# Performance work log

Measured on AMD Instinct MI355X. Metric: run time of the kernel, lower is better.

The kernel has to match this reference:

```python
import jax, jax.numpy as jnp
import numpy as np

O, A, H, L = 32, 8, 256, 3   # obs_units, act_units, hidden_units, hidden_layers
SCALE = 1.0                  # obs_scale
N, W = 512, 128              # n obs/action rows, n hypernet weight samples
W_TOTAL = (O*H + H) + (A*H + H) + (2*H*H + H) + L*(H*H + H) + (H*O + O) + (H + 1) + (H + 1)  # 348194


def _unpack(w):
    # Slice the flat per-sample weight vector exactly as PrimaryNetwork.feedforward does.
    c = [0]
    def take(n, shape=None):
        s = w[:, c[0]:c[0]+n]
        c[0] += n
        return s.reshape((w.shape[0],) + shape) if shape is not None else s
    w_obs = take(O*H, (H, O)); b_obs = take(H)
    w_act = take(A*H, (H, A)); b_act = take(H)
    w_tgt = take(2*H*H, (H, 2*H)); b_tgt = take(H)
    ws, bs = [], []
    for _ in range(L):
        ws.append(take(H*H, (H, H))); bs.append(take(H))
    w_state = take(H*O, (O, H)); b_state = take(O)
    w_reward = take(H, (1, H)); b_reward = take(1)
    w_done = take(H, (1, H)); b_done = take(1)
    return w_obs, b_obs, w_act, b_act, w_tgt, b_tgt, ws, bs, w_state, b_state, w_reward, b_reward, w_done, b_done


def setup_inputs() -> dict:
    key = jax.random.key(0)
    k1, k2, k3 = jax.random.split(key, 3)
    return {
        "obs": jax.random.normal(k1, (N, O), jnp.float32),
        "action": jax.random.normal(k2, (N, A), jnp.float32),
        # scale ~1/sqrt(H) so activations stay in a sane range through the MLP
        "w": jax.random.normal(k3, (W, W_TOTAL), jnp.float32) * (1.0 / np.sqrt(H)),
        "obs_min": jnp.zeros((O,), jnp.float32),
        "obs_max": jnp.ones((O,), jnp.float32),
    }


def reference(obs, action, w, obs_min, obs_max):
    lrelu = jax.nn.leaky_relu  # negative_slope=0.01, matches F.leaky_relu default
    (w_obs, b_obs, w_act, b_act, w_tgt, b_tgt, ws, bs,
     w_state, b_state, w_reward, b_reward, w_done, b_done) = _unpack(w)

    # normalize obs to [-scale, scale]
    x = (obs - obs_min[None, :]) / (obs_max - obs_min)[None, :]
    x = (2.0 * x - 1.0) * SCALE                         # [N, O]

    # per-sample hypernetwork MLP, batched over (N obs rows) x (W weight samples)
    o = jnp.einsum('who,no->nwh', w_obs, x) + b_obs[None]          # [N, W, H]
    a = jnp.einsum('wha,na->nwh', w_act, action) + b_act[None]     # [N, W, H]
    y = lrelu(jnp.concatenate([o, a], axis=-1))                    # [N, W, 2H]
    y = lrelu(jnp.einsum('whk,nwk->nwh', w_tgt, y) + b_tgt[None])  # [N, W, H]
    for wj, bj in zip(ws, bs):
        y = lrelu(jnp.einsum('whk,nwk->nwh', wj, y) + bj[None])

    next_states = jnp.einsum('wok,nwk->nwo', w_state, y) + b_state[None] + x[:, None, :]  # [N, W, O]
    rewards = jnp.tanh(jnp.einsum('wok,nwk->nwo', w_reward, y) + b_reward[None])          # [N, W, 1]
    dones = jax.nn.sigmoid(jnp.einsum('wok,nwk->nwo', w_done, y) + b_done[None])          # [N, W, 1]

    # un-normalize next_states
    next_states = (next_states / SCALE + 1.0) * 0.5
    next_states = next_states * (obs_max - obs_min)[None, None, :] + obs_min[None, None, :]
    return next_states, rewards, dones
```

## Files before the change

kernel.cpp:

```cpp
#include <hip/hip_runtime.h>
#include <cstdint>
#include <cstddef>

#define NMEM    128
#define WTOTAL  348194

#define OFF_WOBS   0
#define OFF_BOBS   8192
#define OFF_WACT   8448
#define OFF_BACT   10496
#define OFF_WTGT   10752
#define OFF_BTGT   141824
#define OFF_WS0    142080
#define OFF_BS0    207616
#define OFF_WS1    207872
#define OFF_BS1    273408
#define OFF_WS2    273664
#define OFF_BS2    339200
#define OFF_WSTATE 339456
#define OFF_BSTATE 347648
#define OFF_WREW   347680
#define OFF_BREW   347936
#define OFF_WDONE  347937
#define OFF_BDONE  348193

#define OUT_REW  2097152
#define OUT_DONE 2162688

#define RB 128
#define APITCH 264

typedef __attribute__((ext_vector_type(8))) short short8;
typedef __attribute__((ext_vector_type(4))) float f32x4;

__device__ __forceinline__ uint32_t pkbf2(float lo, float hi) {
  union { float f; uint32_t u; } a, b;
  a.f = lo; b.f = hi;
  return __builtin_amdgcn_perm(b.u + 0x8000u, a.u + 0x8000u, 0x07060302u);
}

__device__ __forceinline__ uint16_t f2b_fast(float f) {
  union { float f; uint32_t u; } x; x.f = f;
  return (uint16_t)((x.u + 0x8000u) >> 16);
}

__device__ __forceinline__ short8 pk8(const float2 f[4]) {
  union { uint32_t u[4]; short8 s; } r;
#pragma unroll
  for (int i = 0; i < 4; ++i) r.u[i] = pkbf2(f[i].x, f[i].y);
  return r.s;
}

__device__ __forceinline__ void zero8(f32x4 acc[8]) {
#pragma unroll
  for (int r = 0; r < 8; ++r)
#pragma unroll
    for (int j = 0; j < 4; ++j) acc[r][j] = 0.0f;
}

__device__ __forceinline__ void accum_k8(f32x4 acc[8],
                                         const uint16_t* __restrict__ Ab,
                                         const float* __restrict__ wrow) {
  float2 f[2][4];
#pragma unroll
  for (int i = 0; i < 4; ++i)
    f[0][i] = reinterpret_cast<const float2*>(wrow)[i];
#pragma unroll
  for (int kt = 0; kt < 8; ++kt) {
    if (kt < 7) {
#pragma unroll
      for (int i = 0; i < 4; ++i)
        f[(kt + 1) & 1][i] =
            reinterpret_cast<const float2*>(wrow + (kt + 1) * 32)[i];
    }
    const short8 b = pk8(f[kt & 1]);
#pragma unroll
    for (int rt = 0; rt < 8; ++rt) {
      const short8 a =
          *reinterpret_cast<const short8*>(Ab + rt * 16 * APITCH + kt * 32);
      acc[rt] = __builtin_amdgcn_mfma_f32_16x16x32_bf16(a, b, acc[rt], 0, 0, 0);
    }
  }
}

__device__ __forceinline__ void epi_lrelu(const f32x4 acc[8], float bv,
                                          uint16_t* __restrict__ B, int c,
                                          int lg) {
#pragma unroll
  for (int rt = 0; rt < 8; ++rt) {
#pragma unroll
    for (int j = 0; j < 4; ++j) {
      float v = acc[rt][j] + bv;
      v = (v > 0.0f) ? v : 0.01f * v;
      B[(rt * 16 + lg * 4 + j) * APITCH + c] = f2b_fast(v);
    }
  }
}

__global__ void __launch_bounds__(1024, 8)
pn_kernel(const float* __restrict__ obs, const float* __restrict__ action,
          const float* __restrict__ w, const float* __restrict__ omin,
          const float* __restrict__ omax, float* __restrict__ out)
{
  __shared__ __align__(16) uint16_t B1[RB * APITCH];

  const int tid  = threadIdx.x;
  const int lane = tid & 63;
  const int wid  = tid >> 6;
  const int lr   = lane & 15;
  const int lg   = lane >> 4;
  const int c    = wid * 16 + lr;

  const int bid    = blockIdx.x;
  const int xcd    = bid & 7;
  const int j5     = bid >> 3;
  const int member = xcd * 16 + (j5 >> 2);
  const int chunk  = j5 & 3;
  const int n0     = chunk * RB;
  const float* wm  = w + (size_t)member * WTOTAL;

  const uint16_t* Ab = B1 + lr * APITCH + lg * 8;

  {
    float sc[8], of[8];
#pragma unroll
    for (int i = 0; i < 8; ++i) {
      const float mn = omin[lg * 8 + i], mx = omax[lg * 8 + i];
      const float s = 2.0f / (mx - mn);
      sc[i] = s;
      of[i] = -mn * s - 1.0f;
    }
    float2 fb[4];
#pragma unroll
    for (int i = 0; i < 4; ++i)
      fb[i] = reinterpret_cast<const float2*>(wm + OFF_WOBS + c * 32 + lg * 8)[i];
    const short8 b = pk8(fb);
    const float bb = wm[OFF_BOBS + c];
#pragma unroll
    for (int rt = 0; rt < 8; ++rt) {
      const int n = n0 + rt * 16 + lr;
      const float4 x0 = *reinterpret_cast<const float4*>(obs + n * 32 + lg * 8);
      const float4 x1 = *reinterpret_cast<const float4*>(obs + n * 32 + lg * 8 + 4);
      union { uint32_t u[4]; short8 s; } afr;
      afr.u[0] = pkbf2(x0.x * sc[0] + of[0], x0.y * sc[1] + of[1]);
      afr.u[1] = pkbf2(x0.z * sc[2] + of[2], x0.w * sc[3] + of[3]);
      afr.u[2] = pkbf2(x1.x * sc[4] + of[4], x1.y * sc[5] + of[5]);
      afr.u[3] = pkbf2(x1.z * sc[6] + of[6], x1.w * sc[7] + of[7]);
      f32x4 a0 = {0.0f, 0.0f, 0.0f, 0.0f};
      a0 = __builtin_amdgcn_mfma_f32_16x16x32_bf16(afr.s, b, a0, 0, 0, 0);
#pragma unroll
      for (int j = 0; j < 4; ++j) {
        float v = a0[j] + bb;
        v = (v > 0.0f) ? v : 0.01f * v;
        B1[(rt * 16 + lg * 4 + j) * APITCH + c] = f2b_fast(v);
      }
    }
  }
  __syncthreads();

  f32x4 acc[8];
  zero8(acc);

  accum_k8(acc, Ab, wm + OFF_WTGT + c * 512 + lg * 8);
  __syncthreads();

  {
    float2 fb[4];
#pragma unroll
    for (int i = 0; i < 4; ++i)
      fb[i] = reinterpret_cast<const float2*>(wm + OFF_WACT + c * 8 + lg * 8)[i];
    const short8 b = pk8(fb);
    const float bb = wm[OFF_BACT + c];
#pragma unroll
    for (int rt = 0; rt < 8; ++rt) {
      const int n = n0 + rt * 16 + lr;
      union { uint32_t u[4]; short8 s; } afr;
      if (lg == 0) {
        const float4 q0 = *reinterpret_cast<const float4*>(action + n * 8);
        const float4 q1 = *reinterpret_cast<const float4*>(action + n * 8 + 4);
        afr.u[0] = pkbf2(q0.x, q0.y);
        afr.u[1] = pkbf2(q0.z, q0.w);
        afr.u[2] = pkbf2(q1.x, q1.y);
        afr.u[3] = pkbf2(q1.z, q1.w);
      } else {
        afr.u[0] = afr.u[1] = afr.u[2] = afr.u[3] = 0u;
      }
      f32x4 a0 = {0.0f, 0.0f, 0.0f, 0.0f};
      a0 = __builtin_amdgcn_mfma_f32_16x16x32_bf16(afr.s, b, a0, 0, 0, 0);
#pragma unroll
      for (int j = 0; j < 4; ++j) {
        float v = a0[j] + bb;
        v = (v > 0.0f) ? v : 0.01f * v;
        B1[(rt * 16 + lg * 4 + j) * APITCH + c] = f2b_fast(v);
      }
    }
  }
  __syncthreads();

  accum_k8(acc, Ab, wm + OFF_WTGT + c * 512 + 256 + lg * 8);
  __syncthreads();
  epi_lrelu(acc, wm[OFF_BTGT + c], B1, c, lg);
  __syncthreads();

  zero8(acc);
  accum_k8(acc, Ab, wm + OFF_WS0 + c * 256 + lg * 8);
  __syncthreads();
  epi_lrelu(acc, wm[OFF_BS0 + c], B1, c, lg);
  __syncthreads();

  zero8(acc);
  accum_k8(acc, Ab, wm + OFF_WS1 + c * 256 + lg * 8);
  __syncthreads();
  epi_lrelu(acc, wm[OFF_BS1 + c], B1, c, lg);
  __syncthreads();

  zero8(acc);
  accum_k8(acc, Ab, wm + OFF_WS2 + c * 256 + lg * 8);
  __syncthreads();
  epi_lrelu(acc, wm[OFF_BS2 + c], B1, c, lg);
  __syncthreads();

  if (wid < 3) {
    zero8(acc);
#pragma unroll
    for (int kt = 0; kt < 8; ++kt) {
      short8 b;
      if (c < 32) {
        const float* p = wm + OFF_WSTATE + c * 256 + kt * 32 + lg * 8;
        float2 f[4];
#pragma unroll
        for (int i = 0; i < 4; ++i) f[i] = reinterpret_cast<const float2*>(p)[i];
        b = pk8(f);
      } else if (c == 32) {
        const float* p = wm + OFF_WREW + kt * 32 + lg * 8;
        float2 f[4];
#pragma unroll
        for (int i = 0; i < 4; ++i) f[i] = reinterpret_cast<const float2*>(p)[i];
        b = pk8(f);
      } else if (c == 33) {
        const float* p = wm + OFF_WDONE + kt * 32 + lg * 8;
        union { uint32_t u[4]; short8 s; } r;
#pragma unroll
        for (int i = 0; i < 4; ++i) r.u[i] = pkbf2(p[2 * i], p[2 * i + 1]);
        b = r.s;
      } else {
        union { uint32_t u[4]; short8 s; } z;
        z.u[0] = z.u[1] = z.u[2] = z.u[3] = 0u;
        b = z.s;
      }
#pragma unroll
      for (int rt = 0; rt < 8; ++rt) {
        const short8 a =
            *reinterpret_cast<const short8*>(Ab + rt * 16 * APITCH + kt * 32);
        acc[rt] = __builtin_amdgcn_mfma_f32_16x16x32_bf16(a, b, acc[rt], 0, 0, 0);
      }
    }

    if (c < 34) {
#pragma unroll
      for (int rt = 0; rt < 8; ++rt) {
#pragma unroll
        for (int j = 0; j < 4; ++j) {
          const int n = n0 + rt * 16 + lg * 4 + j;
          float v = acc[rt][j];
          if (c < 32) {
            const float mn = omin[c], mx = omax[c];
            const float rng = mx - mn;
            const float x = 2.0f * (obs[n * 32 + c] - mn) / rng - 1.0f;
            v += wm[OFF_BSTATE + c] + x;
            v = (v + 1.0f) * 0.5f;
            out[((size_t)n * NMEM + member) * 32 + c] = v * rng + mn;
          } else if (c == 32) {
            v += wm[OFF_BREW];
            out[(size_t)OUT_REW + (size_t)n * NMEM + member] = tanhf(v);
          } else {
            v += wm[OFF_BDONE];
            out[(size_t)OUT_DONE + (size_t)n * NMEM + member] =
                1.0f / (1.0f + expf(-v));
          }
        }
      }
    }
  }
}

extern "C" void kernel_launch(void* const* d_in, const int* in_sizes, int n_in,
                              void* d_out, int out_size, void* d_ws, size_t ws_size,
                              hipStream_t stream) {
  (void)in_sizes; (void)n_in; (void)out_size; (void)d_ws; (void)ws_size;
  const float* obs    = (const float*)d_in[0];
  const float* action = (const float*)d_in[1];
  const float* w      = (const float*)d_in[2];
  const float* omin   = (const float*)d_in[3];
  const float* omax   = (const float*)d_in[4];
  float* out = (float*)d_out;

  pn_kernel<<<dim3(512), dim3(1024), 0, stream>>>(obs, action, w, omin, omax, out);
}
```

Baseline: 135.7 us.

## Stage hidden-layer weights through double-buffered swizzled LDS with coalesced prefetch

Per-lane strided global loads of weight rows for each MFMA k-step are replaced by a cooperative, coalesced load of 64-wide K slices for all 256 output columns. Each slice is packed to bf16 and written into a double-buffered XOR-swizzled LDS tile, and the next slice (including the next layer's first slice) is prefetched while MFMAs consume the current one. This aims to cut global load inefficiency and latency stalls. In exchange it adds 64KB of LDS, a barrier per slice, and lowers the launch_bounds occupancy hint.

```diff
diff --git a/kernel.cpp b/kernel.cpp
--- a/kernel.cpp
+++ b/kernel.cpp
@@ -29,9 +29,11 @@
 
 #define RB 128
 #define APITCH 264
+#define WSN 16384
 
 typedef __attribute__((ext_vector_type(8))) short short8;
 typedef __attribute__((ext_vector_type(4))) float f32x4;
+typedef __attribute__((ext_vector_type(4))) unsigned int u32x4;
 
 __device__ __forceinline__ uint32_t pkbf2(float lo, float hi) {
   union { float f; uint32_t u; } a, b;
@@ -44,7 +46,7 @@
   return (uint16_t)((x.u + 0x8000u) >> 16);
 }
 
-__device__ __forceinline__ short8 pk8(const float2 f[4]) {
+__device__ __forceinline__ short8 pk8f2(const float2 f[4]) {
   union { uint32_t u[4]; short8 s; } r;
 #pragma unroll
   for (int i = 0; i < 4; ++i) r.u[i] = pkbf2(f[i].x, f[i].y);
@@ -58,28 +60,48 @@
     for (int j = 0; j < 4; ++j) acc[r][j] = 0.0f;
 }
 
-__device__ __forceinline__ void accum_k8(f32x4 acc[8],
-                                         const uint16_t* __restrict__ Ab,
-                                         const float* __restrict__ wrow) {
-  float2 f[2][4];
-#pragma unroll
-  for (int i = 0; i < 4; ++i)
-    f[0][i] = reinterpret_cast<const float2*>(wrow)[i];
-#pragma unroll
-  for (int kt = 0; kt < 8; ++kt) {
-    if (kt < 7) {
-#pragma unroll
-      for (int i = 0; i < 4; ++i)
-        f[(kt + 1) & 1][i] =
-            reinterpret_cast<const float2*>(wrow + (kt + 1) * 32)[i];
-    }
-    const short8 b = pk8(f[kt & 1]);
-#pragma unroll
-    for (int rt = 0; rt < 8; ++rt) {
-      const short8 a =
-          *reinterpret_cast<const short8*>(Ab + rt * 16 * APITCH + kt * 32);
-      acc[rt] = __builtin_amdgcn_mfma_f32_16x16x32_bf16(a, b, acc[rt], 0, 0, 0);
-    }
+__device__ __forceinline__ void ws_commit(const float2 g[8], uint16_t* wsb,
+                                          int wsoff0, int wsoff1) {
+  uint32_t d[8];
+#pragma unroll
+  for (int i = 0; i < 8; ++i) d[i] = pkbf2(g[i].x, g[i].y);
+  *reinterpret_cast<u32x4*>(wsb + wsoff0) = (u32x4){d[0], d[1], d[2], d[3]};
+  *reinterpret_cast<u32x4*>(wsb + wsoff1) = (u32x4){d[4], d[5], d[6], d[7]};
+}
+
+template <bool NX>
+__device__ __forceinline__ void accum_lds(f32x4 acc[8],
+                                          const uint16_t* __restrict__ Ab,
+                                          uint16_t* __restrict__ WS,
+                                          const float* __restrict__ sp,
+                                          const float* __restrict__ np,
+                                          int wsoff0, int wsoff1,
+                                          int wrd, int lrm, int lg) {
+#pragma unroll
+  for (int s = 0; s < 4; ++s) {
+    float2 g[8];
+    if (s < 3 || NX) {
+      const float* src = (s < 3) ? (sp + (s + 1) * 64) : np;
+#pragma unroll
+      for (int i = 0; i < 8; ++i)
+        g[i] = reinterpret_cast<const float2*>(src)[i];
+    }
+    const uint16_t* wsr = WS + (s & 1) * WSN + wrd;
+#pragma unroll
+    for (int h = 0; h < 2; ++h) {
+      const short8 b = *reinterpret_cast<const short8*>(
+          wsr + (((h * 4 + lg) ^ lrm) * 8));
+#pragma unroll
+      for (int rt = 0; rt < 8; ++rt) {
+        const short8 a = *reinterpret_cast<const short8*>(
+            Ab + rt * 16 * APITCH + (s * 2 + h) * 32);
+        acc[rt] =
+            __builtin_amdgcn_mfma_f32_16x16x32_bf16(a, b, acc[rt], 0, 0, 0);
+      }
+    }
+    if (s < 3 || NX)
+      ws_commit(g, WS + ((s + 1) & 1) * WSN, wsoff0, wsoff1);
+    __syncthreads();
   }
 }
 
@@ -97,12 +119,13 @@
   }
 }
 
-__global__ void __launch_bounds__(1024, 8)
+__global__ void __launch_bounds__(1024, 4)
 pn_kernel(const float* __restrict__ obs, const float* __restrict__ action,
           const float* __restrict__ w, const float* __restrict__ omin,
           const float* __restrict__ omax, float* __restrict__ out)
 {
   __shared__ __align__(16) uint16_t B1[RB * APITCH];
+  __shared__ __align__(16) uint16_t WS[2 * WSN];
 
   const int tid  = threadIdx.x;
   const int lane = tid & 63;
@@ -121,6 +144,23 @@
 
   const uint16_t* Ab = B1 + lr * APITCH + lg * 8;
 
+  const int scol   = tid >> 2;
+  const int spart  = tid & 3;
+  const int wsoff0 = scol * 64 + (((2 * spart)     ^ (scol & 7)) * 8);
+  const int wsoff1 = scol * 64 + (((2 * spart + 1) ^ (scol & 7)) * 8);
+  const float* sp_t1 = wm + OFF_WTGT + scol * 512 + spart * 16;
+  const float* sp_t2 = sp_t1 + 256;
+  const float* sp_h0 = wm + OFF_WS0 + scol * 256 + spart * 16;
+  const float* sp_h1 = wm + OFF_WS1 + scol * 256 + spart * 16;
+  const float* sp_h2 = wm + OFF_WS2 + scol * 256 + spart * 16;
+  const int wrd = c * 64;
+  const int lrm = lr & 7;
+
+  float2 gp[8];
+#pragma unroll
+  for (int i = 0; i < 8; ++i)
+    gp[i] = reinterpret_cast<const float2*>(sp_t1)[i];
+
   {
     float sc[8], of[8];
 #pragma unroll
@@ -134,7 +174,7 @@
 #pragma unroll
     for (int i = 0; i < 4; ++i)
       fb[i] = reinterpret_cast<const float2*>(wm + OFF_WOBS + c * 32 + lg * 8)[i];
-    const short8 b = pk8(fb);
+    const short8 b = pk8f2(fb);
     const float bb = wm[OFF_BOBS + c];
 #pragma unroll
     for (int rt = 0; rt < 8; ++rt) {
@@ -156,20 +196,20 @@
       }
     }
   }
+  ws_commit(gp, WS, wsoff0, wsoff1);
   __syncthreads();
 
   f32x4 acc[8];
   zero8(acc);
 
-  accum_k8(acc, Ab, wm + OFF_WTGT + c * 512 + lg * 8);
-  __syncthreads();
+  accum_lds<true>(acc, Ab, WS, sp_t1, sp_t2, wsoff0, wsoff1, wrd, lrm, lg);
 
   {
     float2 fb[4];
 #pragma unroll
     for (int i = 0; i < 4; ++i)
       fb[i] = reinterpret_cast<const float2*>(wm + OFF_WACT + c * 8 + lg * 8)[i];
-    const short8 b = pk8(fb);
+    const short8 b = pk8f2(fb);
     const float bb = wm[OFF_BACT + c];
 #pragma unroll
     for (int rt = 0; rt < 8; ++rt) {
@@ -197,26 +237,22 @@
   }
   __syncthreads();
 
-  accum_k8(acc, Ab, wm + OFF_WTGT + c * 512 + 256 + lg * 8);
-  __syncthreads();
+  accum_lds<true>(acc, Ab, WS, sp_t2, sp_h0, wsoff0, wsoff1, wrd, lrm, lg);
   epi_lrelu(acc, wm[OFF_BTGT + c], B1, c, lg);
   __syncthreads();
 
   zero8(acc);
-  accum_k8(acc, Ab, wm + OFF_WS0 + c * 256 + lg * 8);
-  __syncthreads();
+  accum_lds<true>(acc, Ab, WS, sp_h0, sp_h1, wsoff0, wsoff1, wrd, lrm, lg);
   epi_lrelu(acc, wm[OFF_BS0 + c], B1, c, lg);
   __syncthreads();
 
   zero8(acc);
-  accum_k8(acc, Ab, wm + OFF_WS1 + c * 256 + lg * 8);
-  __syncthreads();
+  accum_lds<true>(acc, Ab, WS, sp_h1, sp_h2, wsoff0, wsoff1, wrd, lrm, lg);
   epi_lrelu(acc, wm[OFF_BS1 + c], B1, c, lg);
   __syncthreads();
 
   zero8(acc);
-  accum_k8(acc, Ab, wm + OFF_WS2 + c * 256 + lg * 8);
-  __syncthreads();
+  accum_lds<false>(acc, Ab, WS, sp_h2, sp_h2, wsoff0, wsoff1, wrd, lrm, lg);
   epi_lrelu(acc, wm[OFF_BS2 + c], B1, c, lg);
   __syncthreads();
 
@@ -230,13 +266,13 @@
         float2 f[4];
 #pragma unroll
         for (int i = 0; i < 4; ++i) f[i] = reinterpret_cast<const float2*>(p)[i];
-        b = pk8(f);
+        b = pk8f2(f);
       } else if (c == 32) {
         const float* p = wm + OFF_WREW + kt * 32 + lg * 8;
         float2 f[4];
 #pragma unroll
         for (int i = 0; i < 4; ++i) f[i] = reinterpret_cast<const float2*>(p)[i];
-        b = pk8(f);
+        b = pk8f2(f);
       } else if (c == 33) {
         const float* p = wm + OFF_WDONE + kt * 32 + lg * 8;
         union { uint32_t u[4]; short8 s; } r;
```

Result: slower. 257.5 us (+89.8%).

## Double row tile to 256 per block and deepen weight prefetch

Applied to the files above, without the earlier changes.

Each block now processes 256 obs rows instead of 128 for one ensemble member, halving the grid to 256 blocks so each member's weights are loaded and converted to bf16 by two blocks rather than four. Accumulators double to 16 MFMA tiles per wave, and the weight loads for a layer are prefetched four k-steps ahead instead of one. The shared activation buffer doubles to about 135 KB and register pressure rises, which lowers occupancy; with 256 blocks there is only one block per CU on a 256-CU part, so latency hiding depends on within-wave ILP.

```diff
diff --git a/kernel.cpp b/kernel.cpp
--- a/kernel.cpp
+++ b/kernel.cpp
@@ -27,7 +27,7 @@
 #define OUT_REW  2097152
 #define OUT_DONE 2162688
 
-#define RB 128
+#define RB 256
 #define APITCH 264
 
 typedef __attribute__((ext_vector_type(8))) short short8;
@@ -44,38 +44,41 @@
   return (uint16_t)((x.u + 0x8000u) >> 16);
 }
 
-__device__ __forceinline__ short8 pk8(const float2 f[4]) {
+__device__ __forceinline__ short8 pk8f2(const float2 f[4]) {
   union { uint32_t u[4]; short8 s; } r;
 #pragma unroll
   for (int i = 0; i < 4; ++i) r.u[i] = pkbf2(f[i].x, f[i].y);
   return r.s;
 }
 
-__device__ __forceinline__ void zero8(f32x4 acc[8]) {
-#pragma unroll
-  for (int r = 0; r < 8; ++r)
+__device__ __forceinline__ void zero16(f32x4 acc[16]) {
+#pragma unroll
+  for (int r = 0; r < 16; ++r)
 #pragma unroll
     for (int j = 0; j < 4; ++j) acc[r][j] = 0.0f;
 }
 
-__device__ __forceinline__ void accum_k8(f32x4 acc[8],
-                                         const uint16_t* __restrict__ Ab,
-                                         const float* __restrict__ wrow) {
-  float2 f[2][4];
-#pragma unroll
-  for (int i = 0; i < 4; ++i)
-    f[0][i] = reinterpret_cast<const float2*>(wrow)[i];
+__device__ __forceinline__ void accum_pass(f32x4 acc[16],
+                                           const uint16_t* __restrict__ Ab,
+                                           const float* __restrict__ w0) {
+  float2 g[4][4];
+#pragma unroll
+  for (int d = 0; d < 4; ++d)
+#pragma unroll
+    for (int i = 0; i < 4; ++i)
+      g[d][i] = reinterpret_cast<const float2*>(w0 + d * 32)[i];
+
 #pragma unroll
   for (int kt = 0; kt < 8; ++kt) {
-    if (kt < 7) {
+    const int s = kt & 3;
+    const short8 b = pk8f2(g[s]);
+    if (kt < 4) {
 #pragma unroll
       for (int i = 0; i < 4; ++i)
-        f[(kt + 1) & 1][i] =
-            reinterpret_cast<const float2*>(wrow + (kt + 1) * 32)[i];
-    }
-    const short8 b = pk8(f[kt & 1]);
-#pragma unroll
-    for (int rt = 0; rt < 8; ++rt) {
+        g[s][i] = reinterpret_cast<const float2*>(w0 + (kt + 4) * 32)[i];
+    }
+#pragma unroll
+    for (int rt = 0; rt < 16; ++rt) {
       const short8 a =
           *reinterpret_cast<const short8*>(Ab + rt * 16 * APITCH + kt * 32);
       acc[rt] = __builtin_amdgcn_mfma_f32_16x16x32_bf16(a, b, acc[rt], 0, 0, 0);
@@ -83,11 +86,11 @@
   }
 }
 
-__device__ __forceinline__ void epi_lrelu(const f32x4 acc[8], float bv,
+__device__ __forceinline__ void epi_lrelu(const f32x4 acc[16], float bv,
                                           uint16_t* __restrict__ B, int c,
                                           int lg) {
 #pragma unroll
-  for (int rt = 0; rt < 8; ++rt) {
+  for (int rt = 0; rt < 16; ++rt) {
 #pragma unroll
     for (int j = 0; j < 4; ++j) {
       float v = acc[rt][j] + bv;
@@ -97,7 +100,7 @@
   }
 }
 
-__global__ void __launch_bounds__(1024, 8)
+__global__ void __launch_bounds__(1024, 4)
 pn_kernel(const float* __restrict__ obs, const float* __restrict__ action,
           const float* __restrict__ w, const float* __restrict__ omin,
           const float* __restrict__ omax, float* __restrict__ out)
@@ -114,8 +117,8 @@
   const int bid    = blockIdx.x;
   const int xcd    = bid & 7;
   const int j5     = bid >> 3;
-  const int member = xcd * 16 + (j5 >> 2);
-  const int chunk  = j5 & 3;
+  const int member = xcd * 16 + (j5 >> 1);
+  const int chunk  = j5 & 1;
   const int n0     = chunk * RB;
   const float* wm  = w + (size_t)member * WTOTAL;
 
@@ -134,10 +137,10 @@
 #pragma unroll
     for (int i = 0; i < 4; ++i)
       fb[i] = reinterpret_cast<const float2*>(wm + OFF_WOBS + c * 32 + lg * 8)[i];
-    const short8 b = pk8(fb);
+    const short8 b = pk8f2(fb);
     const float bb = wm[OFF_BOBS + c];
 #pragma unroll
-    for (int rt = 0; rt < 8; ++rt) {
+    for (int rt = 0; rt < 16; ++rt) {
       const int n = n0 + rt * 16 + lr;
       const float4 x0 = *reinterpret_cast<const float4*>(obs + n * 32 + lg * 8);
       const float4 x1 = *reinterpret_cast<const float4*>(obs + n * 32 + lg * 8 + 4);
@@ -158,10 +161,10 @@
   }
   __syncthreads();
 
-  f32x4 acc[8];
-  zero8(acc);
-
-  accum_k8(acc, Ab, wm + OFF_WTGT + c * 512 + lg * 8);
+  f32x4 acc[16];
+  zero16(acc);
+
+  accum_pass(acc, Ab, wm + OFF_WTGT + c * 512 + lg * 8);
   __syncthreads();
 
   {
@@ -169,10 +172,10 @@
 #pragma unroll
     for (int i = 0; i < 4; ++i)
       fb[i] = reinterpret_cast<const float2*>(wm + OFF_WACT + c * 8 + lg * 8)[i];
-    const short8 b = pk8(fb);
+    const short8 b = pk8f2(fb);
     const float bb = wm[OFF_BACT + c];
 #pragma unroll
-    for (int rt = 0; rt < 8; ++rt) {
+    for (int rt = 0; rt < 16; ++rt) {
       const int n = n0 + rt * 16 + lr;
       union { uint32_t u[4]; short8 s; } afr;
       if (lg == 0) {
@@ -197,31 +200,31 @@
   }
   __syncthreads();
 
-  accum_k8(acc, Ab, wm + OFF_WTGT + c * 512 + 256 + lg * 8);
+  accum_pass(acc, Ab, wm + OFF_WTGT + c * 512 + 256 + lg * 8);
   __syncthreads();
   epi_lrelu(acc, wm[OFF_BTGT + c], B1, c, lg);
   __syncthreads();
 
-  zero8(acc);
-  accum_k8(acc, Ab, wm + OFF_WS0 + c * 256 + lg * 8);
+  zero16(acc);
+  accum_pass(acc, Ab, wm + OFF_WS0 + c * 256 + lg * 8);
   __syncthreads();
   epi_lrelu(acc, wm[OFF_BS0 + c], B1, c, lg);
   __syncthreads();
 
-  zero8(acc);
-  accum_k8(acc, Ab, wm + OFF_WS1 + c * 256 + lg * 8);
+  zero16(acc);
+  accum_pass(acc, Ab, wm + OFF_WS1 + c * 256 + lg * 8);
   __syncthreads();
   epi_lrelu(acc, wm[OFF_BS1 + c], B1, c, lg);
   __syncthreads();
 
-  zero8(acc);
-  accum_k8(acc, Ab, wm + OFF_WS2 + c * 256 + lg * 8);
+  zero16(acc);
+  accum_pass(acc, Ab, wm + OFF_WS2 + c * 256 + lg * 8);
   __syncthreads();
   epi_lrelu(acc, wm[OFF_BS2 + c], B1, c, lg);
   __syncthreads();
 
   if (wid < 3) {
-    zero8(acc);
+    zero16(acc);
 #pragma unroll
     for (int kt = 0; kt < 8; ++kt) {
       short8 b;
@@ -230,13 +233,13 @@
         float2 f[4];
 #pragma unroll
         for (int i = 0; i < 4; ++i) f[i] = reinterpret_cast<const float2*>(p)[i];
-        b = pk8(f);
+        b = pk8f2(f);
       } else if (c == 32) {
         const float* p = wm + OFF_WREW + kt * 32 + lg * 8;
         float2 f[4];
 #pragma unroll
         for (int i = 0; i < 4; ++i) f[i] = reinterpret_cast<const float2*>(p)[i];
-        b = pk8(f);
+        b = pk8f2(f);
       } else if (c == 33) {
         const float* p = wm + OFF_WDONE + kt * 32 + lg * 8;
         union { uint32_t u[4]; short8 s; } r;
@@ -249,7 +252,7 @@
         b = z.s;
       }
 #pragma unroll
-      for (int rt = 0; rt < 8; ++rt) {
+      for (int rt = 0; rt < 16; ++rt) {
         const short8 a =
             *reinterpret_cast<const short8*>(Ab + rt * 16 * APITCH + kt * 32);
         acc[rt] = __builtin_amdgcn_mfma_f32_16x16x32_bf16(a, b, acc[rt], 0, 0, 0);
@@ -258,7 +261,7 @@
 
     if (c < 34) {
 #pragma unroll
-      for (int rt = 0; rt < 8; ++rt) {
+      for (int rt = 0; rt < 16; ++rt) {
 #pragma unroll
         for (int j = 0; j < 4; ++j) {
           const int n = n0 + rt * 16 + lg * 4 + j;
@@ -295,5 +298,5 @@
   const float* omax   = (const float*)d_in[4];
   float* out = (float*)d_out;
 
-  pn_kernel<<<dim3(512), dim3(1024), 0, stream>>>(obs, action, w, omin, omax, out);
-}
+  pn_kernel<<<dim3(256), dim3(1024), 0, stream>>>(obs, action, w, omin, omax, out);
+}
```

Result: faster. 129.7 us (-4.4%).
